# Optimization experiments

Measured on AMD Instinct MI355X. Metric: run time of the kernel, lower is better.

## Reference

```python
import jax, jax.numpy as jnp
import numpy as np


def _avgpool(x, k):
    # x: (N, C, H, W), k divides H and W
    if k == 1:
        return x
    N, C, H, W = x.shape
    return x.reshape(N, C, H // k, k, W // k, k).mean(axis=(3, 5))


def _pairwise_sum(mu1, var1, mu2, var2):
    # mu*, var*: (N, D). Broadcast to (N, N, D), fused elementwise chain + full sum.
    d = mu1[:, None, :] - mu2[None, :, :]
    v = var1[:, None, :] + var2[None, :, :]
    return jnp.sum(jnp.exp(-0.5 * d * d / v) / jnp.sqrt(v))


def setup_inputs() -> dict:
    key = jax.random.key(0)
    k1, k2, k3, k4 = jax.random.split(key, 4)
    shape = (64, 16, 64, 64)
    return {
        "mu_a": jax.random.normal(k1, shape, dtype=jnp.float32),
        "logvar_a": jax.random.normal(k2, shape, dtype=jnp.float32),
        "mu_b": jax.random.normal(k3, shape, dtype=jnp.float32),
        "logvar_b": jax.random.normal(k4, shape, dtype=jnp.float32),
        "kern": 2,
    }


def reference(mu_a, logvar_a, mu_b, logvar_b, kern):
    k2 = float(kern * kern)
    mu_a_p = _avgpool(mu_a, kern)
    mu_b_p = _avgpool(mu_b, kern)
    var_a = _avgpool(jnp.exp(logvar_a), kern) / k2
    var_b = _avgpool(jnp.exp(logvar_b), kern) / k2

    N = mu_a_p.shape[0]
    mu_a_f = mu_a_p.reshape(N, -1)
    mu_b_f = mu_b_p.reshape(N, -1)
    var_a_f = var_a.reshape(N, -1)
    var_b_f = var_b.reshape(N, -1)

    vaa = _pairwise_sum(mu_a_f, var_a_f, mu_a_f, var_a_f)
    vab = _pairwise_sum(mu_a_f, var_a_f, mu_b_f, var_b_f)
    vbb = _pairwise_sum(mu_b_f, var_b_f, mu_b_f, var_b_f)
    return vaa + vbb - 2.0 * vab
```

## Files before the change

kernel.cpp:

```cpp
#include <hip/hip_runtime.h>

#define N_ 64
#define C_ 16
#define H_ 64
#define W_ 64

#define TRI_TILES 72
#define TILES 272
#define DCHUNKS 16
#define PAIR_BLOCKS (TILES * DCHUNKS)

#define TWO_LN2   1.3862943611198906f
#define SQRT_2LN2 1.1774100225154747f


typedef __attribute__((ext_vector_type(2))) float f32x2;

__global__ __launch_bounds__(256) void pool_kernel(
    const float* __restrict__ mu_a, const float* __restrict__ lv_a,
    const float* __restrict__ mu_b, const float* __restrict__ lv_b,
    const int* __restrict__ kern_p, float* __restrict__ ws) {
    const int k = kern_p[0];
    const float LOG2E = 1.44269504088896f;

    if (k == 2) {
        const int Np = (N_ * C_ * H_ * W_) >> 2;
        const int Q  = Np >> 2;
        const int total = 4 * Q;
        for (int g = blockIdx.x * blockDim.x + threadIdx.x; g < total;
             g += gridDim.x * blockDim.x) {
            const int a  = g >> 18;
            const int r4 = g & (Q - 1);
            const int pw4 = (r4 & 7) << 2;
            const int t   = r4 >> 3;
            const int ph  = t & 31;
            const int nc  = t >> 5;
            const float* src = (a == 0) ? mu_a : (a == 1) ? lv_a : (a == 2) ? mu_b : lv_b;
            const bool is_var = (a & 1);
            const float* p0 = src + nc * (H_ * W_) + (ph * 2) * W_ + pw4 * 2;
            float4 r0a = *(const float4*)(p0);
            float4 r0b = *(const float4*)(p0 + 4);
            float4 r1a = *(const float4*)(p0 + W_);
            float4 r1b = *(const float4*)(p0 + W_ + 4);
            float o0, o1, o2, o3;
            if (is_var) {
#define E_(x) __builtin_amdgcn_exp2f((x) * LOG2E)
                o0 = E_(r0a.x) + E_(r0a.y) + E_(r1a.x) + E_(r1a.y);
                o1 = E_(r0a.z) + E_(r0a.w) + E_(r1a.z) + E_(r1a.w);
                o2 = E_(r0b.x) + E_(r0b.y) + E_(r1b.x) + E_(r1b.y);
                o3 = E_(r0b.z) + E_(r0b.w) + E_(r1b.z) + E_(r1b.w);
#undef E_
                const float s = (1.0f / 16.0f) * TWO_LN2;
                o0 *= s; o1 *= s; o2 *= s; o3 *= s;
            } else {
                o0 = r0a.x + r0a.y + r1a.x + r1a.y;
                o1 = r0a.z + r0a.w + r1a.z + r1a.w;
                o2 = r0b.x + r0b.y + r1b.x + r1b.y;
                o3 = r0b.z + r0b.w + r1b.z + r1b.w;
                const float s = 0.25f;
                o0 *= s; o1 *= s; o2 *= s; o3 *= s;
            }
            *(float4*)(ws + (size_t)a * Np + (size_t)r4 * 4) = make_float4(o0, o1, o2, o3);
        }
    } else {
        const int Hp = H_ / k, Wp = W_ / k;
        const int Np = N_ * C_ * Hp * Wp;
        const float inv_k2 = 1.0f / (float)(k * k);
        const float inv_k4 = inv_k2 * inv_k2 * TWO_LN2;
        const int total = 4 * Np;
        for (int p = blockIdx.x * blockDim.x + threadIdx.x; p < total;
             p += gridDim.x * blockDim.x) {
            const int a  = p / Np;
            const int r  = p - a * Np;
            const int pw = r % Wp;
            const int t1 = r / Wp;
            const int ph = t1 % Hp;
            const int nc = t1 / Hp;
            const float* src = (a == 0) ? mu_a : (a == 1) ? lv_a : (a == 2) ? mu_b : lv_b;
            const bool is_var = (a & 1);
            const int base = nc * (H_ * W_) + (ph * k) * W_ + (pw * k);
            float s = 0.0f;
            for (int dy = 0; dy < k; ++dy) {
                const float* row = src + base + dy * W_;
                for (int dx = 0; dx < k; ++dx) {
                    float x = row[dx];
                    s += is_var ? __builtin_amdgcn_exp2f(x * LOG2E) : x;
                }
            }
            ws[(size_t)a * Np + r] = s * (is_var ? inv_k4 : inv_k2);
        }
    }
}

#define TERM2(ACC, IM, IV, JM, JV)                                     \
    {                                                                  \
        f32x2 v_  = (IV) + (JV);                                       \
        f32x2 rs_; rs_.x = __builtin_amdgcn_rsqf(v_.x);                \
                   rs_.y = __builtin_amdgcn_rsqf(v_.y);                \
        f32x2 d_  = (IM) - (JM);                                       \
        f32x2 t_  = d_ * rs_;                                          \
        f32x2 nt_ = -t_ * t_;                                          \
        f32x2 e_; e_.x = __builtin_amdgcn_exp2f(nt_.x);                \
                  e_.y = __builtin_amdgcn_exp2f(nt_.y);                \
        ACC += e_ * rs_;                                               \
    }

__global__ __launch_bounds__(256) void pair_kernel(float* __restrict__ ws,
                                                   const int* __restrict__ kern_p) {
    const int k = kern_p[0];
    const int D  = C_ * (H_ / k) * (W_ / k);
    const int Np = N_ * D;

    const float* mu_a = ws;
    const float* va   = ws + (size_t)Np;
    const float* mu_b = ws + (size_t)2 * Np;
    const float* vb   = ws + (size_t)3 * Np;
    float* partials   = ws + (size_t)4 * Np;

    const int c = blockIdx.x & (DCHUNKS - 1);
    const int t = blockIdx.x >> 4;
    int set, it, jt;
    if (t >= 2 * TRI_TILES) {
        set = 2;
        const int tt = t - 2 * TRI_TILES;
        it = tt >> 3;
        jt = tt & 7;
    } else {
        set = (t >= TRI_TILES) ? 1 : 0;
        const int tt = set ? (t - TRI_TILES) : t;
        int g = 0, cum = 0;
        while (cum + (g >> 1) + 1 <= tt) { cum += (g >> 1) + 1; ++g; }
        it = g;
        jt = tt - cum;
    }
    const int i0 = it * 4, j0 = jt * 8;

    const float *mu1, *v1, *mu2, *v2;
    if (set == 0)      { mu1 = mu2 = mu_a; v1 = v2 = va; }
    else if (set == 1) { mu1 = mu2 = mu_b; v1 = v2 = vb; }
    else               { mu1 = mu_a; v1 = va; mu2 = mu_b; v2 = vb; }

    const bool uniform = (set == 2) || (jt < (it >> 1));
    const float wU = (set == 2) ? -2.0f : 2.0f;

    float tot = 0.0f;

    if (D == 16384) {
        const int base = (c << 10) + ((int)threadIdx.x << 2);
        f32x2 imlo[4], imhi[4], ivlo[4], ivhi[4];
        #pragma unroll
        for (int ir = 0; ir < 4; ++ir) {
            const float4 m4 = *(const float4*)(mu1 + (size_t)(i0 + ir) * 16384 + base);
            const float4 v4 = *(const float4*)(v1  + (size_t)(i0 + ir) * 16384 + base);
            imlo[ir].x = m4.x; imlo[ir].y = m4.y; imhi[ir].x = m4.z; imhi[ir].y = m4.w;
            ivlo[ir].x = v4.x; ivlo[ir].y = v4.y; ivhi[ir].x = v4.z; ivhi[ir].y = v4.w;
        }
        if (uniform) {
            f32x2 acc2[4];
            #pragma unroll
            for (int ir = 0; ir < 4; ++ir) { acc2[ir].x = 0.0f; acc2[ir].y = 0.0f; }
            #pragma unroll
            for (int j8 = 0; j8 < 8; ++j8) {
                const float4 jm = *(const float4*)(mu2 + (size_t)(j0 + j8) * 16384 + base);
                const float4 jv = *(const float4*)(v2  + (size_t)(j0 + j8) * 16384 + base);
                f32x2 jmlo, jmhi, jvlo, jvhi;
                jmlo.x = jm.x; jmlo.y = jm.y; jmhi.x = jm.z; jmhi.y = jm.w;
                jvlo.x = jv.x; jvlo.y = jv.y; jvhi.x = jv.z; jvhi.y = jv.w;
                #pragma unroll
                for (int ir = 0; ir < 4; ++ir) {
                    TERM2(acc2[ir], imlo[ir], ivlo[ir], jmlo, jvlo)
                    TERM2(acc2[ir], imhi[ir], ivhi[ir], jmhi, jvhi)
                }
            }
            const f32x2 s2 = (acc2[0] + acc2[1]) + (acc2[2] + acc2[3]);
            tot = wU * (s2.x + s2.y);
        } else {
            #pragma unroll
            for (int j8 = 0; j8 < 8; ++j8) {
                const float4 jm = *(const float4*)(mu2 + (size_t)(j0 + j8) * 16384 + base);
                const float4 jv = *(const float4*)(v2  + (size_t)(j0 + j8) * 16384 + base);
                f32x2 jmlo, jmhi, jvlo, jvhi;
                jmlo.x = jm.x; jmlo.y = jm.y; jmhi.x = jm.z; jmhi.y = jm.w;
                jvlo.x = jv.x; jvlo.y = jv.y; jvhi.x = jv.z; jvhi.y = jv.w;
                const int jj = j0 + j8;
                #pragma unroll
                for (int ir = 0; ir < 4; ++ir) {
                    f32x2 a; a.x = 0.0f; a.y = 0.0f;
                    TERM2(a, imlo[ir], ivlo[ir], jmlo, jvlo)
                    TERM2(a, imhi[ir], ivhi[ir], jmhi, jvhi)
                    const int ii = i0 + ir;
                    const float w = (jj > ii) ? 0.0f : (jj == ii) ? 1.0f : 2.0f;
                    tot = fmaf(w, a.x + a.y, tot);
                }
            }
        }
    } else {
        const int cs = D / DCHUNKS;
        const int lo = c * cs, hi = lo + cs;
        for (int e = lo + (int)threadIdx.x; e < hi; e += 256) {
            #pragma unroll
            for (int j8 = 0; j8 < 8; ++j8) {
                const int jj = j0 + j8;
                const float mj = mu2[(size_t)jj * D + e];
                const float vj = v2 [(size_t)jj * D + e];
                #pragma unroll
                for (int ir = 0; ir < 4; ++ir) {
                    const int ii = i0 + ir;
                    const float w = (set == 2) ? -2.0f
                                  : (jj > ii) ? 0.0f : (jj == ii) ? 1.0f : 2.0f;
                    const float mi = mu1[(size_t)ii * D + e];
                    const float vi = v1 [(size_t)ii * D + e];
                    float v_  = vi + vj;
                    float rs_ = __builtin_amdgcn_rsqf(v_);
                    float d_  = mi - mj;
                    float t_  = d_ * rs_;
                    float e_  = __builtin_amdgcn_exp2f(-(t_ * t_));
                    tot = fmaf(w, e_ * rs_, tot);
                }
            }
        }
    }

    tot *= SQRT_2LN2;

    for (int off = 32; off > 0; off >>= 1)
        tot += __shfl_down(tot, off, 64);
    __shared__ float wsum[4];
    const int lane = threadIdx.x & 63;
    const int wid  = threadIdx.x >> 6;
    if (lane == 0) wsum[wid] = tot;
    __syncthreads();
    if (threadIdx.x == 0) {
        partials[blockIdx.x] = wsum[0] + wsum[1] + wsum[2] + wsum[3];
    }
}

__global__ __launch_bounds__(256) void reduce_kernel(const float* __restrict__ ws,
                                                     const int* __restrict__ kern_p,
                                                     float* __restrict__ out) {
    const int k = kern_p[0];
    const int D  = C_ * (H_ / k) * (W_ / k);
    const int Np = N_ * D;
    const float* partials = ws + (size_t)4 * Np;

    float s = 0.0f;
    for (int p = threadIdx.x; p < PAIR_BLOCKS; p += 256) s += partials[p];
    for (int off = 32; off > 0; off >>= 1)
        s += __shfl_down(s, off, 64);
    __shared__ float wsum[4];
    const int lane = threadIdx.x & 63;
    const int wid  = threadIdx.x >> 6;
    if (lane == 0) wsum[wid] = s;
    __syncthreads();
    if (threadIdx.x == 0) out[0] = wsum[0] + wsum[1] + wsum[2] + wsum[3];
}

extern "C" void kernel_launch(void* const* d_in, const int* in_sizes, int n_in,
                              void* d_out, int out_size, void* d_ws, size_t ws_size,
                              hipStream_t stream) {
    const float* mu_a = (const float*)d_in[0];
    const float* lv_a = (const float*)d_in[1];
    const float* mu_b = (const float*)d_in[2];
    const float* lv_b = (const float*)d_in[3];
    const int*   kern = (const int*)d_in[4];
    float* out = (float*)d_out;
    float* ws  = (float*)d_ws;

    pool_kernel<<<4096, 256, 0, stream>>>(mu_a, lv_a, mu_b, lv_b, kern, ws);
    pair_kernel<<<PAIR_BLOCKS, 256, 0, stream>>>(ws, kern);
    reduce_kernel<<<1, 256, 0, stream>>>(ws, kern, out);
}
```

Measured before the change: 136.2 us.

## Double-buffer j-row loads through LDS with async global_load_lds

Replaces the direct global float4 loads of the j rows in the pair kernel with asynchronous global-to-LDS copies (global_load_lds, 16 bytes per lane) into a two-stage LDS buffer. Each iteration prefetches the next j row while computing on the current one, using manual s_waitcnt vmcnt. The goal is to hide global load latency behind the exp/rsq arithmetic. The uniform and diagonal paths are merged into one loop with a branch inside. It relies on the LDS destination layout of per-wave global_load_lds matching the tid<<2 read pattern, and it omits explicit barriers. Its correctness therefore depends on each wave reading only its own region.

```diff
diff --git a/kernel.cpp b/kernel.cpp
--- a/kernel.cpp
+++ b/kernel.cpp
@@ -92,6 +92,12 @@
     }
 }
 
+__device__ __forceinline__ void g2lds16(const float* g, float* l) {
+    __builtin_amdgcn_global_load_lds(
+        (const __attribute__((address_space(1))) void*)g,
+        (__attribute__((address_space(3))) void*)l, 16, 0, 0);
+}
+
 #define TERM2(ACC, IM, IV, JM, JV)                                     \
     {                                                                  \
         f32x2 v_  = (IV) + (JV);                                       \
@@ -116,6 +122,8 @@
     const float* mu_b = ws + (size_t)2 * Np;
     const float* vb   = ws + (size_t)3 * Np;
     float* partials   = ws + (size_t)4 * Np;
+
+    __shared__ float jbuf[2][2][1024];
 
     const int c = blockIdx.x & (DCHUNKS - 1);
     const int t = blockIdx.x >> 4;
@@ -146,7 +154,17 @@
     float tot = 0.0f;
 
     if (D == 16384) {
-        const int base = (c << 10) + ((int)threadIdx.x << 2);
+        const int tid  = (int)threadIdx.x;
+        const int wq   = (tid >> 6) << 8;
+        const int base = (c << 10) + (tid << 2);
+        const float* gjm = mu2 + (size_t)j0 * 16384 + base;
+        const float* gjv = v2  + (size_t)j0 * 16384 + base;
+
+#define STAGE(J8, BUF)                                        \
+        { g2lds16(gjm + (size_t)(J8) * 16384, &jbuf[BUF][0][wq]); \
+          g2lds16(gjv + (size_t)(J8) * 16384, &jbuf[BUF][1][wq]); }
+
+        STAGE(0, 0)
         f32x2 imlo[4], imhi[4], ivlo[4], ivhi[4];
         #pragma unroll
         for (int ir = 0; ir < 4; ++ir) {
@@ -155,33 +173,34 @@
             imlo[ir].x = m4.x; imlo[ir].y = m4.y; imhi[ir].x = m4.z; imhi[ir].y = m4.w;
             ivlo[ir].x = v4.x; ivlo[ir].y = v4.y; ivhi[ir].x = v4.z; ivhi[ir].y = v4.w;
         }
-        if (uniform) {
-            f32x2 acc2[4];
-            #pragma unroll
-            for (int ir = 0; ir < 4; ++ir) { acc2[ir].x = 0.0f; acc2[ir].y = 0.0f; }
-            #pragma unroll
-            for (int j8 = 0; j8 < 8; ++j8) {
-                const float4 jm = *(const float4*)(mu2 + (size_t)(j0 + j8) * 16384 + base);
-                const float4 jv = *(const float4*)(v2  + (size_t)(j0 + j8) * 16384 + base);
-                f32x2 jmlo, jmhi, jvlo, jvhi;
-                jmlo.x = jm.x; jmlo.y = jm.y; jmhi.x = jm.z; jmhi.y = jm.w;
-                jvlo.x = jv.x; jvlo.y = jv.y; jvhi.x = jv.z; jvhi.y = jv.w;
+
+        f32x2 acc2[4];
+        #pragma unroll
+        for (int ir = 0; ir < 4; ++ir) { acc2[ir].x = 0.0f; acc2[ir].y = 0.0f; }
+
+        #pragma unroll
+        for (int j8 = 0; j8 < 8; ++j8) {
+            if (j8 < 7) {
+                STAGE(j8 + 1, (j8 + 1) & 1)
+                asm volatile("s_waitcnt vmcnt(2)" ::: "memory");
+            } else {
+                asm volatile("s_waitcnt vmcnt(0)" ::: "memory");
+            }
+            __builtin_amdgcn_sched_barrier(0);
+
+            const float4 jm = *(const float4*)&jbuf[j8 & 1][0][tid << 2];
+            const float4 jv = *(const float4*)&jbuf[j8 & 1][1][tid << 2];
+            f32x2 jmlo, jmhi, jvlo, jvhi;
+            jmlo.x = jm.x; jmlo.y = jm.y; jmhi.x = jm.z; jmhi.y = jm.w;
+            jvlo.x = jv.x; jvlo.y = jv.y; jvhi.x = jv.z; jvhi.y = jv.w;
+
+            if (uniform) {
                 #pragma unroll
                 for (int ir = 0; ir < 4; ++ir) {
                     TERM2(acc2[ir], imlo[ir], ivlo[ir], jmlo, jvlo)
                     TERM2(acc2[ir], imhi[ir], ivhi[ir], jmhi, jvhi)
                 }
-            }
-            const f32x2 s2 = (acc2[0] + acc2[1]) + (acc2[2] + acc2[3]);
-            tot = wU * (s2.x + s2.y);
-        } else {
-            #pragma unroll
-            for (int j8 = 0; j8 < 8; ++j8) {
-                const float4 jm = *(const float4*)(mu2 + (size_t)(j0 + j8) * 16384 + base);
-                const float4 jv = *(const float4*)(v2  + (size_t)(j0 + j8) * 16384 + base);
-                f32x2 jmlo, jmhi, jvlo, jvhi;
-                jmlo.x = jm.x; jmlo.y = jm.y; jmhi.x = jm.z; jmhi.y = jm.w;
-                jvlo.x = jv.x; jvlo.y = jv.y; jvhi.x = jv.z; jvhi.y = jv.w;
+            } else {
                 const int jj = j0 + j8;
                 #pragma unroll
                 for (int ir = 0; ir < 4; ++ir) {
@@ -193,6 +212,11 @@
                     tot = fmaf(w, a.x + a.y, tot);
                 }
             }
+        }
+#undef STAGE
+        if (uniform) {
+            const f32x2 s2 = (acc2[0] + acc2[1]) + (acc2[2] + acc2[3]);
+            tot = wU * (s2.x + s2.y);
         }
     } else {
         const int cs = D / DCHUNKS;
```

Result: no change. 138.5 us (+1.7%).

## Enlarge pair tiles to 16x8 with LDS-staged i-rows via direct global-to-LDS loads

Applied to the files above, without the earlier changes.

The pair tile grows from 4x8 to 16x8 samples and the feature dimension is split into 32 chunks of 512 instead of 16 of 1024. The 8 j-rows stay in registers, and the 16 i-rows are staged into shared memory with global_load_lds direct loads. The goal is to cut redundant global and L2 traffic per pair term and to shrink the wasted work in the triangular tiles of the symmetric sets. In exchange the kernel uses 64KB of LDS per block, which limits occupancy, adds a barrier, and launches fewer blocks (2304 instead of 4352).

```diff
diff --git a/kernel.cpp b/kernel.cpp
--- a/kernel.cpp
+++ b/kernel.cpp
@@ -5,9 +5,10 @@
 #define H_ 64
 #define W_ 64
 
-#define TRI_TILES 72
-#define TILES 272
-#define DCHUNKS 16
+#define TRI_TILES 20
+#define TILES 72
+#define DCHUNKS 32
+#define CHUNK 512
 #define PAIR_BLOCKS (TILES * DCHUNKS)
 
 #define TWO_LN2   1.3862943611198906f
@@ -92,6 +93,12 @@
     }
 }
 
+__device__ __forceinline__ void g2lds16(const float* g, float* l) {
+    __builtin_amdgcn_global_load_lds(
+        (const __attribute__((address_space(1))) void*)g,
+        (__attribute__((address_space(3))) void*)l, 16, 0, 0);
+}
+
 #define TERM2(ACC, IM, IV, JM, JV)                                     \
     {                                                                  \
         f32x2 v_  = (IV) + (JV);                                       \
@@ -117,8 +124,10 @@
     const float* vb   = ws + (size_t)3 * Np;
     float* partials   = ws + (size_t)4 * Np;
 
+    __shared__ float ilds[16][2][CHUNK];
+
     const int c = blockIdx.x & (DCHUNKS - 1);
-    const int t = blockIdx.x >> 4;
+    const int t = blockIdx.x >> 5;
     int set, it, jt;
     if (t >= 2 * TRI_TILES) {
         set = 2;
@@ -129,93 +138,107 @@
         set = (t >= TRI_TILES) ? 1 : 0;
         const int tt = set ? (t - TRI_TILES) : t;
         int g = 0, cum = 0;
-        while (cum + (g >> 1) + 1 <= tt) { cum += (g >> 1) + 1; ++g; }
+        while (cum + 2 * g + 2 <= tt) { cum += 2 * g + 2; ++g; }
         it = g;
         jt = tt - cum;
     }
-    const int i0 = it * 4, j0 = jt * 8;
+    const int i0 = it * 16, j0 = jt * 8;
 
     const float *mu1, *v1, *mu2, *v2;
     if (set == 0)      { mu1 = mu2 = mu_a; v1 = v2 = va; }
     else if (set == 1) { mu1 = mu2 = mu_b; v1 = v2 = vb; }
     else               { mu1 = mu_a; v1 = va; mu2 = mu_b; v2 = vb; }
 
-    const bool uniform = (set == 2) || (jt < (it >> 1));
+    const bool uniform = (set == 2) || (jt < 2 * it);
     const float wU = (set == 2) ? -2.0f : 2.0f;
 
+    const int tid  = (int)threadIdx.x;
+    const int lane = tid & 63;
+    const int wid  = tid >> 6;
+
     float tot = 0.0f;
 
     if (D == 16384) {
-        const int base = (c << 10) + ((int)threadIdx.x << 2);
-        f32x2 imlo[4], imhi[4], ivlo[4], ivhi[4];
+        const int ebase = (c << 9) + (tid << 1);
+
+        f32x2 jm[8], jv[8];
         #pragma unroll
-        for (int ir = 0; ir < 4; ++ir) {
-            const float4 m4 = *(const float4*)(mu1 + (size_t)(i0 + ir) * 16384 + base);
-            const float4 v4 = *(const float4*)(v1  + (size_t)(i0 + ir) * 16384 + base);
-            imlo[ir].x = m4.x; imlo[ir].y = m4.y; imhi[ir].x = m4.z; imhi[ir].y = m4.w;
-            ivlo[ir].x = v4.x; ivlo[ir].y = v4.y; ivhi[ir].x = v4.z; ivhi[ir].y = v4.w;
-        }
+        for (int j8 = 0; j8 < 8; ++j8) {
+            jm[j8] = *(const f32x2*)(mu2 + (size_t)(j0 + j8) * 16384 + ebase);
+            jv[j8] = *(const f32x2*)(v2  + (size_t)(j0 + j8) * 16384 + ebase);
+        }
+
+        {
+            const int lbase = (c << 9) + (lane << 2);
+            #pragma unroll
+            for (int q = 0; q < 8; ++q) {
+                const int p   = (wid << 3) | q;
+                const int row = p >> 1;
+                const int arr = p & 1;
+                const float* g0 = (arr ? v1 : mu1) + (size_t)(i0 + row) * 16384 + lbase;
+                g2lds16(g0,       &ilds[row][arr][0]);
+                g2lds16(g0 + 256, &ilds[row][arr][256]);
+            }
+        }
+        __syncthreads();
+
         if (uniform) {
-            f32x2 acc2[4];
-            #pragma unroll
-            for (int ir = 0; ir < 4; ++ir) { acc2[ir].x = 0.0f; acc2[ir].y = 0.0f; }
-            #pragma unroll
-            for (int j8 = 0; j8 < 8; ++j8) {
-                const float4 jm = *(const float4*)(mu2 + (size_t)(j0 + j8) * 16384 + base);
-                const float4 jv = *(const float4*)(v2  + (size_t)(j0 + j8) * 16384 + base);
-                f32x2 jmlo, jmhi, jvlo, jvhi;
-                jmlo.x = jm.x; jmlo.y = jm.y; jmhi.x = jm.z; jmhi.y = jm.w;
-                jvlo.x = jv.x; jvlo.y = jv.y; jvhi.x = jv.z; jvhi.y = jv.w;
+            f32x2 a0; a0.x = 0.0f; a0.y = 0.0f;
+            f32x2 a1; a1.x = 0.0f; a1.y = 0.0f;
+            #pragma unroll 2
+            for (int ir = 0; ir < 16; ++ir) {
+                const f32x2 imu = *(const f32x2*)&ilds[ir][0][tid << 1];
+                const f32x2 ivv = *(const f32x2*)&ilds[ir][1][tid << 1];
                 #pragma unroll
-                for (int ir = 0; ir < 4; ++ir) {
-                    TERM2(acc2[ir], imlo[ir], ivlo[ir], jmlo, jvlo)
-                    TERM2(acc2[ir], imhi[ir], ivhi[ir], jmhi, jvhi)
-                }
-            }
-            const f32x2 s2 = (acc2[0] + acc2[1]) + (acc2[2] + acc2[3]);
+                for (int j8 = 0; j8 < 8; ++j8) {
+                    TERM2(((j8 & 1) ? a1 : a0), imu, ivv, jm[j8], jv[j8])
+                }
+            }
+            const f32x2 s2 = a0 + a1;
             tot = wU * (s2.x + s2.y);
         } else {
-            #pragma unroll
-            for (int j8 = 0; j8 < 8; ++j8) {
-                const float4 jm = *(const float4*)(mu2 + (size_t)(j0 + j8) * 16384 + base);
-                const float4 jv = *(const float4*)(v2  + (size_t)(j0 + j8) * 16384 + base);
-                f32x2 jmlo, jmhi, jvlo, jvhi;
-                jmlo.x = jm.x; jmlo.y = jm.y; jmhi.x = jm.z; jmhi.y = jm.w;
-                jvlo.x = jv.x; jvlo.y = jv.y; jvhi.x = jv.z; jvhi.y = jv.w;
-                const int jj = j0 + j8;
+            float t0 = 0.0f, t1 = 0.0f;
+            #pragma unroll 2
+            for (int ir = 0; ir < 16; ++ir) {
+                const f32x2 imu = *(const f32x2*)&ilds[ir][0][tid << 1];
+                const f32x2 ivv = *(const f32x2*)&ilds[ir][1][tid << 1];
+                const int ii = i0 + ir;
                 #pragma unroll
-                for (int ir = 0; ir < 4; ++ir) {
+                for (int j8 = 0; j8 < 8; ++j8) {
                     f32x2 a; a.x = 0.0f; a.y = 0.0f;
-                    TERM2(a, imlo[ir], ivlo[ir], jmlo, jvlo)
-                    TERM2(a, imhi[ir], ivhi[ir], jmhi, jvhi)
-                    const int ii = i0 + ir;
+                    TERM2(a, imu, ivv, jm[j8], jv[j8])
+                    const int jj = j0 + j8;
                     const float w = (jj > ii) ? 0.0f : (jj == ii) ? 1.0f : 2.0f;
-                    tot = fmaf(w, a.x + a.y, tot);
-                }
-            }
+                    if (j8 & 1) t1 = fmaf(w, a.x + a.y, t1);
+                    else        t0 = fmaf(w, a.x + a.y, t0);
+                }
+            }
+            tot = t0 + t1;
         }
     } else {
-        const int cs = D / DCHUNKS;
-        const int lo = c * cs, hi = lo + cs;
-        for (int e = lo + (int)threadIdx.x; e < hi; e += 256) {
-            #pragma unroll
-            for (int j8 = 0; j8 < 8; ++j8) {
-                const int jj = j0 + j8;
-                const float mj = mu2[(size_t)jj * D + e];
-                const float vj = v2 [(size_t)jj * D + e];
+        const int cs = (D >= DCHUNKS) ? (D / DCHUNKS) : 1;
+        const int lo = c * cs;
+        if (lo < D) {
+            const int hi = (lo + cs < D) ? (lo + cs) : D;
+            for (int e = lo + tid; e < hi; e += 256) {
                 #pragma unroll
-                for (int ir = 0; ir < 4; ++ir) {
-                    const int ii = i0 + ir;
-                    const float w = (set == 2) ? -2.0f
-                                  : (jj > ii) ? 0.0f : (jj == ii) ? 1.0f : 2.0f;
-                    const float mi = mu1[(size_t)ii * D + e];
-                    const float vi = v1 [(size_t)ii * D + e];
-                    float v_  = vi + vj;
-                    float rs_ = __builtin_amdgcn_rsqf(v_);
-                    float d_  = mi - mj;
-                    float t_  = d_ * rs_;
-                    float e_  = __builtin_amdgcn_exp2f(-(t_ * t_));
-                    tot = fmaf(w, e_ * rs_, tot);
+                for (int j8 = 0; j8 < 8; ++j8) {
+                    const int jj = j0 + j8;
+                    const float mj = mu2[(size_t)jj * D + e];
+                    const float vj = v2 [(size_t)jj * D + e];
+                    for (int ir = 0; ir < 16; ++ir) {
+                        const int ii = i0 + ir;
+                        const float w = (set == 2) ? -2.0f
+                                      : (jj > ii) ? 0.0f : (jj == ii) ? 1.0f : 2.0f;
+                        const float mi = mu1[(size_t)ii * D + e];
+                        const float vi = v1 [(size_t)ii * D + e];
+                        float v_  = vi + vj;
+                        float rs_ = __builtin_amdgcn_rsqf(v_);
+                        float d_  = mi - mj;
+                        float t_  = d_ * rs_;
+                        float e_  = __builtin_amdgcn_exp2f(-(t_ * t_));
+                        tot = fmaf(w, e_ * rs_, tot);
+                    }
                 }
             }
         }
@@ -225,12 +248,11 @@
 
     for (int off = 32; off > 0; off >>= 1)
         tot += __shfl_down(tot, off, 64);
-    __shared__ float wsum[4];
-    const int lane = threadIdx.x & 63;
-    const int wid  = threadIdx.x >> 6;
+    __syncthreads();
+    float* wsum = &ilds[0][0][0];
     if (lane == 0) wsum[wid] = tot;
     __syncthreads();
-    if (threadIdx.x == 0) {
+    if (tid == 0) {
         partials[blockIdx.x] = wsum[0] + wsum[1] + wsum[2] + wsum[3];
     }
 }
```

Result: slower. 142.8 us (+4.9%).
